# Optimization experiments

Measured on AMD Instinct MI355X. Metric: run time of the kernel, lower is better.

Reference implementation:

```python
import jax, jax.numpy as jnp
import numpy as np


def segment_pool(labels, hidden):
    """Faithful vectorized version of get_entity_embedding_from_hidden_states.

    labels: [B, L] int (0=O, 1=B, 2=I); hidden: [B, L, H].
    Returns [B, L, H]: per-row, the first count_ones(row) slots hold the mean
    hidden state of each mention segment (segments delimited by label==1 over
    the nonzero-label token stream, flattened across the whole batch), rest 0.
    """
    B, L, H = hidden.shape
    N = B * L
    lab = labels.reshape(N)
    h = hidden.reshape(N, H)
    m = lab != 0
    # stable sort: nonzero-label tokens first, original order preserved
    perm = jnp.argsort(jnp.logical_not(m))
    lab_s = lab[perm]
    h_s = h[perm]
    m_s = m[perm]
    b = (lab_s == 1).astype(jnp.int32)
    cum = jnp.cumsum(b)                      # ones seen so far (nonzero stream)
    idx0 = jnp.argmax(b)                     # position of first B-tag (0 if none)
    p = jnp.arange(N)
    # chunk id of nonzero-stream token p: (#ones at positions <= p+idx0) - 1
    seg = cum[jnp.minimum(p + idx0, N - 1)] - 1
    valid = m_s & (seg >= 0)
    seg_ids = jnp.where(valid, seg, N)       # invalid tokens -> dumped segment N
    sums = jax.ops.segment_sum(h_s, seg_ids, num_segments=N + 1)[:N]
    counts = jax.ops.segment_sum(valid.astype(h.dtype), seg_ids, num_segments=N + 1)[:N]
    means = sums / jnp.maximum(counts, 1.0)[:, None]   # [N, H]
    # re-split per row: row b consumes count_ones(b) consecutive means, padded to L
    c = jnp.sum(labels == 1, axis=1)         # [B]
    starts = jnp.cumsum(c) - c               # exclusive prefix sum
    j = jnp.arange(L)
    gidx = jnp.clip(starts[:, None] + j[None, :], 0, N - 1)  # [B, L]
    out = means[gidx]                        # [B, L, H]
    return jnp.where((j[None, :] < c[:, None])[:, :, None], out, jnp.zeros((), hidden.dtype))


def setup_inputs() -> dict:
    key = jax.random.key(0)
    ks = jax.random.split(key, 8)
    B, L, H, E, P = 64, 512, 768, 1000, 300
    return {
        "bio_slot_labels": jax.random.randint(ks[0], (B, L), 0, 3, dtype=jnp.int32),
        "hidden_states": jax.random.normal(ks[1], (B, L, H), dtype=jnp.float32),
        "entity_type_embeddings": jax.random.normal(ks[2], (E, H), dtype=jnp.float32),
        "w1": jax.random.normal(ks[3], (H, H), dtype=jnp.float32) * 0.02,
        "b1": jnp.zeros((H,), dtype=jnp.float32),
        "w2": jax.random.normal(ks[4], (H, 3), dtype=jnp.float32) * 0.02,
        "b2": jnp.zeros((3,), dtype=jnp.float32),
        "w_mention": jax.random.normal(ks[5], (H, P), dtype=jnp.float32) * 0.02,
        "w_desc": jax.random.normal(ks[6], (H, P), dtype=jnp.float32) * 0.02,
    }


def reference(bio_slot_labels, hidden_states, entity_type_embeddings,
              w1, b1, w2, b2, w_mention, w_desc):
    # bio_mlp: Linear -> ReLU -> Linear -> LogSoftmax
    h1 = jax.nn.relu(jnp.einsum('blh,hk->blk', hidden_states, w1) + b1)
    bio_slot_logits = jax.nn.log_softmax(jnp.einsum('blh,hc->blc', h1, w2) + b2, axis=-1)
    predicted_bio_slot = jnp.argmax(bio_slot_logits, axis=-1)

    proj_desc = entity_type_embeddings @ w_desc          # [E, 300]

    def score(labels):
        pooled = segment_pool(labels, hidden_states)     # [B, L, H]
        proj_mention = jnp.einsum('blh,hp->blp', pooled, w_mention)
        dot = jnp.einsum('blp,ep->ble', proj_mention, proj_desc)
        return jax.nn.log_softmax(dot, axis=-1)

    return (bio_slot_logits, score(bio_slot_labels), score(predicted_bio_slot))
```

## Files before the change

kernel.cpp:

```cpp
#include <hip/hip_runtime.h>
#include <stdint.h>

__device__ inline float bf2f(unsigned short u) { return __uint_as_float(((unsigned int)u) << 16); }
__device__ inline unsigned short f2bf(float f) {
    unsigned int x = __float_as_uint(f);
    unsigned int r = x + 0x7fffu + ((x >> 16) & 1u);
    return (unsigned short)(r >> 16);
}

typedef __attribute__((ext_vector_type(8))) short bf16x8;
typedef __attribute__((ext_vector_type(4))) float f32x4;
typedef __attribute__((ext_vector_type(4))) int   v4i;
typedef __attribute__((ext_vector_type(4))) unsigned short u16x4;

#define FLAG_CAP 8192
#define MARGIN 0.02

__device__ inline void gload16(const void* g, void* l) {
    __builtin_amdgcn_global_load_lds(
        (const __attribute__((address_space(1))) void*)g,
        (__attribute__((address_space(3))) void*)l, 16, 0, 0);
}

__global__ __launch_bounds__(256) void gemm_bt(
    const unsigned short* __restrict__ A,
    const unsigned short* __restrict__ Bt,
    void* __restrict__ C,
    const int* __restrict__ Mdev,
    const int* __restrict__ rowMap,
    const float* __restrict__ fb1,
    const float* __restrict__ fw2,
    float* __restrict__ fpart,
    int M, int N, int K, int lda, int ldb, int ldc, int mode, int rowOff,
    size_t zA, int zMeta, int zMap, size_t zC)
{
    int zz = blockIdx.z;
    A += (size_t)zz * zA;
    if (Mdev) M = Mdev[zz * zMeta];
    if (rowMap) rowMap += (size_t)zz * zMap;

    int NT = gridDim.x;
    int p  = blockIdx.x + NT * blockIdx.y;
    int i8 = p >> 3;
    int mt = (p & 7) + 8 * (i8 / NT);
    int nt = i8 % NT;

    if (rowOff + mt * 128 >= M) return;

    __shared__ __align__(16) unsigned short As[128 * 64];
    __shared__ __align__(16) unsigned short Bs[128 * 64];

    int tid  = threadIdx.x;
    int lane = tid & 63, wave = tid >> 6;
    int wRow = (wave >> 1) * 64, wCol = (wave & 1) * 64;
    int mBase = mt * 128, nBase = nt * 128;
    int lm = lane & 15, kg = lane >> 4;
    int sr = tid >> 3;
    int sc = (tid & 7) * 8;

    f32x4 acc[4][4] = {};

    for (int k0 = 0; k0 < K; k0 += 64) {
        __syncthreads();
#pragma unroll
        for (int i = 0; i < 4; ++i) {
            int r = sr + 32 * i;
            int gm = rowOff + mBase + r; if (gm > M - 1) gm = M - 1;
            gload16(&A[(size_t)(gm - rowOff) * lda + k0 + sc], &As[wave * 512 + i * 2048]);
            int gn = nBase + r; if (gn > N - 1) gn = N - 1;
            gload16(&Bt[(size_t)gn * ldb + k0 + sc], &Bs[wave * 512 + i * 2048]);
        }
        __syncthreads();
#pragma unroll
        for (int ks = 0; ks < 2; ++ks) {
            bf16x8 af[4], bfr[4];
#pragma unroll
            for (int i = 0; i < 4; ++i) {
                af[i]  = *(const bf16x8*)&As[(wRow + i * 16 + lm) * 64 + ks * 32 + kg * 8];
                bfr[i] = *(const bf16x8*)&Bs[(wCol + i * 16 + lm) * 64 + ks * 32 + kg * 8];
            }
#pragma unroll
            for (int mi = 0; mi < 4; ++mi)
#pragma unroll
                for (int ni = 0; ni < 4; ++ni)
                    acc[mi][ni] = __builtin_amdgcn_mfma_f32_16x16x32_bf16(
                        af[mi], bfr[ni], acc[mi][ni], 0, 0, 0);
        }
    }

    int rbase = (lane >> 4) * 4;

    if (mode == 3) {
        float b1v[4], w2l[4][3];
#pragma unroll
        for (int ni = 0; ni < 4; ++ni) {
            int n = nBase + wCol + ni * 16 + lm;
            b1v[ni] = fb1[n];
#pragma unroll
            for (int c = 0; c < 3; ++c) w2l[ni][c] = fw2[n * 3 + c];
        }
#pragma unroll
        for (int mi = 0; mi < 4; ++mi) {
            float p2[4][3] = {};
#pragma unroll
            for (int ni = 0; ni < 4; ++ni)
#pragma unroll
                for (int r = 0; r < 4; ++r) {
                    float v = acc[mi][ni][r] + b1v[ni];
                    v = fmaxf(v, 0.f);
                    p2[r][0] += v * w2l[ni][0];
                    p2[r][1] += v * w2l[ni][1];
                    p2[r][2] += v * w2l[ni][2];
                }
#pragma unroll
            for (int r = 0; r < 4; ++r)
#pragma unroll
                for (int c = 0; c < 3; ++c) {
                    float s = p2[r][c];
                    s += __shfl_down(s, 8); s += __shfl_down(s, 4);
                    s += __shfl_down(s, 2); s += __shfl_down(s, 1);
                    p2[r][c] = s;
                }
            if (lm == 0) {
#pragma unroll
                for (int r = 0; r < 4; ++r) {
                    int row = mBase + wRow + mi * 16 + rbase + r;
#pragma unroll
                    for (int c = 0; c < 3; ++c)
                        atomicAdd(&fpart[(size_t)row * 3 + c], p2[r][c]);
                }
            }
        }
        return;
    }

#pragma unroll
    for (int mi = 0; mi < 4; ++mi) {
#pragma unroll
        for (int r = 0; r < 4; ++r) {
            int m = rowOff + mBase + wRow + mi * 16 + rbase + r;
            if (m >= M) continue;
            size_t crow = rowMap ? (size_t)rowMap[m] * ldc : (size_t)(m - rowOff) * ldc;
#pragma unroll
            for (int ni = 0; ni < 4; ++ni) {
                int n = nBase + wCol + ni * 16 + lm;
                if (n >= N) continue;
                float v = acc[mi][ni][r];
                if (mode == 2) ((float*)C)[(size_t)zz * zC + crow + n] = v;
                else           ((unsigned short*)C)[crow + n] = f2bf(v);
            }
        }
    }
}

__global__ __launch_bounds__(256) void prep_all(
    const float* __restrict__ ent, unsigned short* __restrict__ entB,
    const float* __restrict__ hidden, unsigned short* __restrict__ hiddenB,
    const float* __restrict__ wd, unsigned short* __restrict__ wdT,
    const float* __restrict__ w1, unsigned short* __restrict__ w1T,
    const float* __restrict__ wm, unsigned short* __restrict__ wmP,
    v4i* __restrict__ zreg)
{
    __shared__ float tile[32][33];
    int b = blockIdx.x, t = threadIdx.x;
    if (b < 373) {
        int i = b * 256 + t;
        if (i < 95312) { v4i z = {0, 0, 0, 0}; zreg[i] = z; }
        return;
    }
    b -= 373;
    if (b < 750) {
        int i = b * 256 + t;
        float4 v = ((const float4*)ent)[i];
        u16x4 o = { f2bf(v.x), f2bf(v.y), f2bf(v.z), f2bf(v.w) };
        ((u16x4*)entB)[i] = o;
        return;
    }
    b -= 750;
    if (b < 24576) {
        int i = b * 256 + t;
        float4 v = ((const float4*)hidden)[i];
        u16x4 o = { f2bf(v.x), f2bf(v.y), f2bf(v.z), f2bf(v.w) };
        ((u16x4*)hiddenB)[i] = o;
        return;
    }
    b -= 24576;
    if (b < 240 + 576) {
        const float* in; unsigned short* out; int R, C, bx, by;
        if (b < 240) { in = wd; out = wdT; R = 768; C = 300; bx = b % 10; by = b / 10; }
        else { int bb = b - 240; in = w1; out = w1T; R = 768; C = 768; bx = bb % 24; by = bb / 24; }
        int tx = t & 31, ty = t >> 5;
        int c0 = bx * 32, r0 = by * 32;
#pragma unroll
        for (int i = 0; i < 4; ++i) {
            int r = r0 + ty + i * 8, c = c0 + tx;
            if (r < R && c < C) tile[ty + i * 8][tx] = in[(size_t)r * C + c];
        }
        __syncthreads();
#pragma unroll
        for (int i = 0; i < 4; ++i) {
            int orow = c0 + ty + i * 8, ocol = r0 + tx;
            if (orow < C && ocol < R) out[(size_t)orow * R + ocol] = f2bf(tile[tx][ty + i * 8]);
        }
        return;
    }
    b -= 816;
    {
        int idx = b * 256 + t;
        if (idx < 768 * 300) wmP[(size_t)(idx / 300) * 320 + (idx % 300)] = f2bf(wm[idx]);
    }
}

__global__ void bio_final2(const float* __restrict__ part, const float* __restrict__ b2,
                           float* __restrict__ out0, int* __restrict__ predLab,
                           int* __restrict__ flagCnt, int* __restrict__ flagList)
{
    int t = blockIdx.x * 256 + threadIdx.x;
    double a[3];
#pragma unroll
    for (int c = 0; c < 3; ++c) a[c] = (double)part[(size_t)t * 3 + c] + (double)b2[c];
    double mx = a[0]; if (a[1] > mx) mx = a[1]; if (a[2] > mx) mx = a[2];
    double ls = mx + log(exp(a[0] - mx) + exp(a[1] - mx) + exp(a[2] - mx));
    out0[t * 3 + 0] = (float)(a[0] - ls);
    out0[t * 3 + 1] = (float)(a[1] - ls);
    out0[t * 3 + 2] = (float)(a[2] - ls);
    int pbest = 0; double bv = a[0];
    if (a[1] > bv) { bv = a[1]; pbest = 1; }
    if (a[2] > bv) { bv = a[2]; pbest = 2; }
    predLab[t] = pbest;
    double second = -1e300;
#pragma unroll
    for (int c = 0; c < 3; ++c) if (c != pbest && a[c] > second) second = a[c];
    if (bv - second < MARGIN) {
        int i = atomicAdd(flagCnt, 1);
        if (i < FLAG_CAP) flagList[i] = t;
    }
}

__global__ __launch_bounds__(256) void h1_bio_gemm(
    const float* __restrict__ hidden, const int* __restrict__ flagList,
    const float* __restrict__ W,
    const float* __restrict__ b1, const float* __restrict__ w2,
    float* __restrict__ part, const int* __restrict__ Mdev, int partStride)
{
    int M = *Mdev; if (M > FLAG_CAP) M = FLAG_CAP;
    if (M <= 0) return;
    int m0 = blockIdx.x * 64, n0 = blockIdx.y * 64;
    if (m0 >= M) return;
    __shared__ float AsT[16][64];
    __shared__ float Ws[16][64];
    int tx = threadIdx.x, ty = threadIdx.y;
    int tid = ty * 16 + tx;
    float acc[4][4] = {};

    for (int k0 = 0; k0 < 768; k0 += 16) {
        __syncthreads();
        {
            int row = tid >> 2, seg = (tid & 3) * 4;
            int gm = m0 + row; if (gm > M - 1) gm = M - 1;
            float4 v = *(const float4*)&hidden[(size_t)flagList[gm] * 768 + k0 + seg];
            AsT[seg + 0][row] = v.x; AsT[seg + 1][row] = v.y;
            AsT[seg + 2][row] = v.z; AsT[seg + 3][row] = v.w;
        }
        {
            int row = tid >> 4, seg = (tid & 15) * 4;
            *(float4*)&Ws[row][seg] = *(const float4*)&W[(size_t)(k0 + row) * 768 + n0 + seg];
        }
        __syncthreads();
#pragma unroll
        for (int kk = 0; kk < 16; ++kk) {
            float4 av = *(const float4*)&AsT[kk][ty * 4];
            float4 bv = *(const float4*)&Ws[kk][tx * 4];
            float a[4] = {av.x, av.y, av.z, av.w};
            float b[4] = {bv.x, bv.y, bv.z, bv.w};
#pragma unroll
            for (int i = 0; i < 4; ++i)
#pragma unroll
                for (int j = 0; j < 4; ++j)
                    acc[i][j] += a[i] * b[j];
        }
    }

    float b1v[4], w2l[4][3];
#pragma unroll
    for (int j = 0; j < 4; ++j) {
        int n = n0 + tx * 4 + j;
        b1v[j] = b1[n];
#pragma unroll
        for (int c = 0; c < 3; ++c) w2l[j][c] = w2[n * 3 + c];
    }
    float p[4][3] = {};
#pragma unroll
    for (int i = 0; i < 4; ++i)
#pragma unroll
        for (int j = 0; j < 4; ++j) {
            float v = acc[i][j] + b1v[j];
            v = fmaxf(v, 0.f);
#pragma unroll
            for (int c = 0; c < 3; ++c) p[i][c] += v * w2l[j][c];
        }
#pragma unroll
    for (int i = 0; i < 4; ++i)
#pragma unroll
        for (int c = 0; c < 3; ++c) {
            float s = p[i][c];
            s += __shfl_down(s, 8); s += __shfl_down(s, 4);
            s += __shfl_down(s, 2); s += __shfl_down(s, 1);
            p[i][c] = s;
        }
    if (tx == 0) {
#pragma unroll
        for (int i = 0; i < 4; ++i) {
            int t = m0 + ty * 4 + i;
            if (t >= M) continue;
#pragma unroll
            for (int c = 0; c < 3; ++c)
                part[(size_t)blockIdx.y * partStride + (size_t)t * 3 + c] = p[i][c];
        }
    }
}

__global__ __launch_bounds__(1024) void seg_prep2(
    const int* __restrict__ labels, int* predLab,
    int* __restrict__ streamTok, int* __restrict__ cumArr,
    int* __restrict__ meta, int* __restrict__ rowC, int* __restrict__ mapArr,
    int* __restrict__ segFirst,
    const float* __restrict__ partF, const float* __restrict__ b2,
    const int* __restrict__ flagList, const int* __restrict__ flagCnt, int partStride)
{
    int setz = blockIdx.x;
    int t = threadIdx.x;

    if (setz == 1) {
        int cnt = *flagCnt; if (cnt > FLAG_CAP) cnt = FLAG_CAP;
        for (int i = t; i < cnt; i += 1024) {
            double a[3] = {(double)b2[0], (double)b2[1], (double)b2[2]};
#pragma unroll
            for (int blk = 0; blk < 12; ++blk)
#pragma unroll
                for (int c = 0; c < 3; ++c)
                    a[c] += (double)partF[(size_t)blk * partStride + (size_t)i * 3 + c];
            int pbest = 0; double bv = a[0];
            if (a[1] > bv) { bv = a[1]; pbest = 1; }
            if (a[2] > bv) { bv = a[2]; pbest = 2; }
            predLab[flagList[i]] = pbest;
        }
        __syncthreads();
    }

    const int* lab = setz ? predLab : labels;
    int* sTok = streamTok + setz * 32768;
    int* sCum = cumArr + setz * 32768;
    int* mt   = meta + setz * 64;
    int* rC   = rowC + setz * 64;
    int* mp   = mapArr + setz * 32768;
    int* sf   = segFirst + setz * 32768;

    __shared__ int sM[1024], sB[1024];
    __shared__ int sRowC[64], sRowStart[64];
    __shared__ int sIdx0;
    if (t == 0) sIdx0 = 0x7fffffff;
    int base = t * 32;
    int vals[32];
#pragma unroll
    for (int j = 0; j < 8; ++j) {
        v4i v = ((const v4i*)lab)[t * 8 + j];
        vals[4 * j + 0] = v[0]; vals[4 * j + 1] = v[1];
        vals[4 * j + 2] = v[2]; vals[4 * j + 3] = v[3];
    }
    int mc = 0, bc = 0;
#pragma unroll
    for (int i = 0; i < 32; ++i) { mc += (vals[i] != 0); bc += (vals[i] == 1); }
    sM[t] = mc; sB[t] = bc; __syncthreads();
    for (int off = 1; off < 1024; off <<= 1) {
        int vm = 0, vb = 0;
        if (t >= off) { vm = sM[t - off]; vb = sB[t - off]; }
        __syncthreads();
        sM[t] += vm; sB[t] += vb;
        __syncthreads();
    }
    int mBase = sM[t] - mc, bBase = sB[t] - bc;
    int mRun = 0, bRun = 0;
#pragma unroll
    for (int i = 0; i < 32; ++i) {
        int v = vals[i];
        if (v != 0) {
            int q = mBase + mRun;
            sTok[q] = base + i;
            int isB = (v == 1);
            sCum[q] = bBase + bRun + isB;
            if (isB && (bBase + bRun) == 0) sIdx0 = q;
            mRun += 1; bRun += isB;
        }
    }
    if ((t & 15) == 0) sRowStart[t >> 4] = bBase;
    __syncthreads();
    if ((t & 15) == 0) {
        int b = t >> 4;
        sRowC[b] = sB[t + 15] - sRowStart[b];
        rC[b] = sRowC[b];
    }
    if (t == 1023) { mt[0] = sB[1023]; mt[1] = sM[1023]; }
    if (t == 0) mt[2] = (sIdx0 == 0x7fffffff) ? 0 : sIdx0;
    __syncthreads();
    for (int idx = t; idx < 32768; idx += 1024) {
        int b = idx >> 9, j = idx & 511;
        if (j < sRowC[b]) mp[sRowStart[b] + j] = idx;
    }

    int K = sM[1023], numB = sB[1023];
    int idx0 = (sIdx0 == 0x7fffffff) ? 0 : sIdx0;
    for (int q = t; q < K; q += 1024) {
        int qq = q + idx0;
        int c  = (qq < K) ? sCum[qq] : numB;
        int sg = c - 1;
        if (sg < 0) continue;
        int sp = -1;
        if (q > 0) {
            int qq2 = qq - 1;
            int c2  = (qq2 < K) ? sCum[qq2] : numB;
            sp = c2 - 1;
        }
        if (sg != sp) sf[sg] = q;
    }
}

__global__ __launch_bounds__(192) void seg_means2(
    const unsigned short* __restrict__ hiddenB, const int* __restrict__ streamTok,
    const int* __restrict__ segFirst, const int* __restrict__ meta,
    unsigned short* __restrict__ means, size_t zMeans)
{
    int setz = blockIdx.y;
    const int* mt = meta + setz * 64;
    int s = blockIdx.x;
    int numB = mt[0];
    if (s >= numB) return;
    const int* st = streamTok + setz * 32768;
    const int* sf = segFirst + setz * 32768;
    int q0 = sf[s];
    int q1 = (s + 1 < numB) ? sf[s + 1] : mt[1];
    int cnt = q1 - q0;
    int t = threadIdx.x;
    float a0 = 0.f, a1 = 0.f, a2 = 0.f, a3 = 0.f;
    for (int i = 0; i < cnt; ++i) {
        const unsigned short* hr = hiddenB + (size_t)st[q0 + i] * 768;
        u16x4 v = *(const u16x4*)&hr[t * 4];
        a0 += bf2f(v[0]); a1 += bf2f(v[1]); a2 += bf2f(v[2]); a3 += bf2f(v[3]);
    }
    float fc = (float)cnt;
    u16x4 o = { f2bf(a0 / fc), f2bf(a1 / fc), f2bf(a2 / fc), f2bf(a3 / fc) };
    *(u16x4*)&means[(size_t)setz * zMeans + (size_t)s * 768 + t * 4] = o;
}

__global__ __launch_bounds__(256) void softmax_rows2(float* __restrict__ outBase,
                                                     const int* __restrict__ rowCBase,
                                                     size_t zC)
{
    float* out = outBase + (size_t)blockIdx.y * zC;
    const int* rowC = rowCBase + blockIdx.y * 64;
    int v = blockIdx.x;
    int b = v >> 9, j = v & 511;
    int t = threadIdx.x;
    float* row = out + (size_t)v * 1000;
    if (j >= rowC[b]) {
        for (int e = t; e < 1000; e += 256) row[e] = -6.907755278982137f;
        return;
    }
    __shared__ float red[256];
    float x0 = row[t];
    float x1 = row[t + 256];
    float x2 = row[t + 512];
    bool has3 = (t + 768) < 1000;
    float x3 = has3 ? row[t + 768] : -1e30f;
    float mx = fmaxf(fmaxf(x0, x1), fmaxf(x2, x3));
    red[t] = mx; __syncthreads();
    for (int st = 128; st > 0; st >>= 1) { if (t < st) red[t] = fmaxf(red[t], red[t + st]); __syncthreads(); }
    float M = red[0]; __syncthreads();
    float sm = expf(x0 - M) + expf(x1 - M) + expf(x2 - M) + (has3 ? expf(x3 - M) : 0.f);
    red[t] = sm; __syncthreads();
    for (int st = 128; st > 0; st >>= 1) { if (t < st) red[t] += red[t + st]; __syncthreads(); }
    float ls = M + logf(red[0]);
    row[t]       = x0 - ls;
    row[t + 256] = x1 - ls;
    row[t + 512] = x2 - ls;
    if (has3) row[t + 768] = x3 - ls;
}

extern "C" void kernel_launch(void* const* d_in, const int* in_sizes, int n_in,
                              void* d_out, int out_size, void* d_ws, size_t ws_size,
                              hipStream_t stream)
{
    (void)in_sizes; (void)n_in; (void)out_size; (void)ws_size;
    const int*   labels = (const int*)d_in[0];
    const float* hidden = (const float*)d_in[1];
    const float* ent    = (const float*)d_in[2];
    const float* w1     = (const float*)d_in[3];
    const float* b1     = (const float*)d_in[4];
    const float* w2     = (const float*)d_in[5];
    const float* b2     = (const float*)d_in[6];
    const float* wm     = (const float*)d_in[7];
    const float* wd     = (const float*)d_in[8];

    char* ws = (char*)d_ws;
    size_t off = 0;
    auto alloc = [&](size_t bytes) {
        void* p = ws + off;
        off = (off + bytes + 255) & ~(size_t)255;
        return p;
    };
    int* meta      = (int*)alloc(512);
    int* rowC      = (int*)alloc(512);
    int* predLab   = (int*)alloc(32768 * 4);
    int* streamTok = (int*)alloc(2 * 32768 * 4);
    int* cumArr    = (int*)alloc(2 * 32768 * 4);
    int* segFirst  = (int*)alloc(2 * 32768 * 4);
    int* mapArr    = (int*)alloc(2 * 32768 * 4);
    int* flagList  = (int*)alloc(FLAG_CAP * 4);
    unsigned short* entB = (unsigned short*)alloc((size_t)1000 * 768 * 2);
    unsigned short* wdT  = (unsigned short*)alloc((size_t)300 * 768 * 2);
    unsigned short* W2t  = (unsigned short*)alloc((size_t)1000 * 768 * 2);
    unsigned short* w1T  = (unsigned short*)alloc((size_t)768 * 768 * 2);
    unsigned short* hiddenB = (unsigned short*)alloc((size_t)32768 * 768 * 2);
    float* partF = (float*)alloc((size_t)12 * FLAG_CAP * 3 * 4);
    char* zbase = (char*)alloc(1524992);
    unsigned short* pd  = (unsigned short*)zbase;
    unsigned short* wmP = (unsigned short*)(zbase + 640000);
    float* part         = (float*)(zbase + 1131520);
    int* flagCnt        = (int*)(zbase + 1524736);
    unsigned short* means = (unsigned short*)alloc((size_t)2 * 32768 * 768 * 2);

    float* out0 = (float*)d_out;
    float* out1 = out0 + 98304;

    prep_all<<<27415, 256, 0, stream>>>(ent, entB, hidden, hiddenB, wd, wdT,
                                        w1, w1T, wm, wmP, (v4i*)zbase);

    gemm_bt<<<dim3(3, 8), 256, 0, stream>>>(entB, wdT, pd, nullptr, nullptr,
                                            nullptr, nullptr, nullptr,
                                            1000, 300, 768, 768, 768, 320, 0, 0,
                                            0, 0, 0, 0);
    gemm_bt<<<dim3(6, 8), 256, 0, stream>>>(pd, wmP, W2t, nullptr, nullptr,
                                            nullptr, nullptr, nullptr,
                                            1000, 768, 320, 320, 320, 768, 0, 0,
                                            0, 0, 0, 0);

    gemm_bt<<<dim3(6, 256), 256, 0, stream>>>(hiddenB, w1T, nullptr, nullptr, nullptr,
                                              b1, w2, part,
                                              32768, 768, 768, 768, 768, 0, 3, 0,
                                              0, 0, 0, 0);
    bio_final2<<<128, 256, 0, stream>>>(part, b2, out0, predLab, flagCnt, flagList);
    h1_bio_gemm<<<dim3(FLAG_CAP / 64, 12), dim3(16, 16), 0, stream>>>(
        hidden, flagList, w1, b1, w2, partF, flagCnt, FLAG_CAP * 3);

    seg_prep2<<<2, 1024, 0, stream>>>(labels, predLab, streamTok, cumArr, meta, rowC,
                                      mapArr, segFirst, partF, b2, flagList, flagCnt,
                                      FLAG_CAP * 3);
    seg_means2<<<dim3(32768, 2), 192, 0, stream>>>(hiddenB, streamTok, segFirst, meta,
                                                   means, (size_t)32768 * 768);
    gemm_bt<<<dim3(8, 256, 2), 256, 0, stream>>>(means, W2t, out1, meta, mapArr,
                                                 nullptr, nullptr, nullptr,
                                                 0, 1000, 768, 768, 768, 1000, 2, 0,
                                                 (size_t)32768 * 768, 64, 32768,
                                                 (size_t)32768 * 1000);
    softmax_rows2<<<dim3(32768, 2), 256, 0, stream>>>(out1, rowC, (size_t)32768 * 1000);
}
```

Before: 807.7 us.

## Merge independent stages into combined launches with block-range dispatch

```diff
diff --git a/kernel.cpp b/kernel.cpp
--- a/kernel.cpp
+++ b/kernel.cpp
@@ -22,7 +22,7 @@
         (__attribute__((address_space(3))) void*)l, 16, 0, 0);
 }
 
-__global__ __launch_bounds__(256) void gemm_bt(
+static __device__ void dev_gemm(
     const unsigned short* __restrict__ A,
     const unsigned short* __restrict__ Bt,
     void* __restrict__ C,
@@ -31,24 +31,12 @@
     const float* __restrict__ fb1,
     const float* __restrict__ fw2,
     float* __restrict__ fpart,
-    int M, int N, int K, int lda, int ldb, int ldc, int mode, int rowOff,
-    size_t zA, int zMeta, int zMap, size_t zC)
-{
-    int zz = blockIdx.z;
-    A += (size_t)zz * zA;
-    if (Mdev) M = Mdev[zz * zMeta];
-    if (rowMap) rowMap += (size_t)zz * zMap;
-
-    int NT = gridDim.x;
-    int p  = blockIdx.x + NT * blockIdx.y;
-    int i8 = p >> 3;
-    int mt = (p & 7) + 8 * (i8 / NT);
-    int nt = i8 % NT;
-
-    if (rowOff + mt * 128 >= M) return;
-
-    __shared__ __align__(16) unsigned short As[128 * 64];
-    __shared__ __align__(16) unsigned short Bs[128 * 64];
+    int M, int N, int K, int lda, int ldb, int ldc, int mode,
+    int mt, int nt,
+    unsigned short* As, unsigned short* Bs)
+{
+    if (Mdev) M = *Mdev;
+    if (mt * 128 >= M) return;
 
     int tid  = threadIdx.x;
     int lane = tid & 63, wave = tid >> 6;
@@ -65,8 +53,8 @@
 #pragma unroll
         for (int i = 0; i < 4; ++i) {
             int r = sr + 32 * i;
-            int gm = rowOff + mBase + r; if (gm > M - 1) gm = M - 1;
-            gload16(&A[(size_t)(gm - rowOff) * lda + k0 + sc], &As[wave * 512 + i * 2048]);
+            int gm = mBase + r; if (gm > M - 1) gm = M - 1;
+            gload16(&A[(size_t)gm * lda + k0 + sc], &As[wave * 512 + i * 2048]);
             int gn = nBase + r; if (gn > N - 1) gn = N - 1;
             gload16(&Bt[(size_t)gn * ldb + k0 + sc], &Bs[wave * 512 + i * 2048]);
         }
@@ -138,84 +126,116 @@
     for (int mi = 0; mi < 4; ++mi) {
 #pragma unroll
         for (int r = 0; r < 4; ++r) {
-            int m = rowOff + mBase + wRow + mi * 16 + rbase + r;
+            int m = mBase + wRow + mi * 16 + rbase + r;
             if (m >= M) continue;
-            size_t crow = rowMap ? (size_t)rowMap[m] * ldc : (size_t)(m - rowOff) * ldc;
+            size_t crow = rowMap ? (size_t)rowMap[m] * ldc : (size_t)m * ldc;
 #pragma unroll
             for (int ni = 0; ni < 4; ++ni) {
                 int n = nBase + wCol + ni * 16 + lm;
                 if (n >= N) continue;
                 float v = acc[mi][ni][r];
-                if (mode == 2) ((float*)C)[(size_t)zz * zC + crow + n] = v;
+                if (mode == 2) ((float*)C)[crow + n] = v;
                 else           ((unsigned short*)C)[crow + n] = f2bf(v);
             }
         }
     }
 }
 
-__global__ __launch_bounds__(256) void prep_all(
-    const float* __restrict__ ent, unsigned short* __restrict__ entB,
-    const float* __restrict__ hidden, unsigned short* __restrict__ hiddenB,
-    const float* __restrict__ wd, unsigned short* __restrict__ wdT,
-    const float* __restrict__ w1, unsigned short* __restrict__ w1T,
-    const float* __restrict__ wm, unsigned short* __restrict__ wmP,
-    v4i* __restrict__ zreg)
-{
-    __shared__ float tile[32][33];
-    int b = blockIdx.x, t = threadIdx.x;
-    if (b < 373) {
-        int i = b * 256 + t;
-        if (i < 95312) { v4i z = {0, 0, 0, 0}; zreg[i] = z; }
-        return;
-    }
-    b -= 373;
-    if (b < 750) {
-        int i = b * 256 + t;
-        float4 v = ((const float4*)ent)[i];
-        u16x4 o = { f2bf(v.x), f2bf(v.y), f2bf(v.z), f2bf(v.w) };
-        ((u16x4*)entB)[i] = o;
-        return;
-    }
-    b -= 750;
-    if (b < 24576) {
-        int i = b * 256 + t;
-        float4 v = ((const float4*)hidden)[i];
-        u16x4 o = { f2bf(v.x), f2bf(v.y), f2bf(v.z), f2bf(v.w) };
-        ((u16x4*)hiddenB)[i] = o;
-        return;
-    }
-    b -= 24576;
-    if (b < 240 + 576) {
-        const float* in; unsigned short* out; int R, C, bx, by;
-        if (b < 240) { in = wd; out = wdT; R = 768; C = 300; bx = b % 10; by = b / 10; }
-        else { int bb = b - 240; in = w1; out = w1T; R = 768; C = 768; bx = bb % 24; by = bb / 24; }
-        int tx = t & 31, ty = t >> 5;
-        int c0 = bx * 32, r0 = by * 32;
-#pragma unroll
-        for (int i = 0; i < 4; ++i) {
-            int r = r0 + ty + i * 8, c = c0 + tx;
-            if (r < R && c < C) tile[ty + i * 8][tx] = in[(size_t)r * C + c];
-        }
-        __syncthreads();
-#pragma unroll
-        for (int i = 0; i < 4; ++i) {
-            int orow = c0 + ty + i * 8, ocol = r0 + tx;
-            if (orow < C && ocol < R) out[(size_t)orow * R + ocol] = f2bf(tile[tx][ty + i * 8]);
-        }
-        return;
-    }
-    b -= 816;
-    {
-        int idx = b * 256 + t;
-        if (idx < 768 * 300) wmP[(size_t)(idx / 300) * 320 + (idx % 300)] = f2bf(wm[idx]);
-    }
-}
-
-__global__ void bio_final2(const float* __restrict__ part, const float* __restrict__ b2,
-                           float* __restrict__ out0, int* __restrict__ predLab,
-                           int* __restrict__ flagCnt, int* __restrict__ flagList)
-{
-    int t = blockIdx.x * 256 + threadIdx.x;
+static __device__ void dev_scan(const int* __restrict__ lab,
+    int* __restrict__ sTok, int* __restrict__ sCum, int* __restrict__ mt,
+    int* __restrict__ rC, int* __restrict__ mp, int* __restrict__ sf,
+    int* sM, int* sB, int* sRS, int* sRC, int* sIdx)
+{
+    int t = threadIdx.x;
+    if (t == 0) sIdx[0] = 0x7fffffff;
+    int mc = 0, bc = 0;
+#pragma unroll
+    for (int j = 0; j < 32; ++j) {
+        v4i v = ((const v4i*)lab)[t * 32 + j];
+#pragma unroll
+        for (int e = 0; e < 4; ++e) { mc += (v[e] != 0); bc += (v[e] == 1); }
+    }
+    sM[t] = mc; sB[t] = bc; __syncthreads();
+    for (int off = 1; off < 256; off <<= 1) {
+        int vm = 0, vb = 0;
+        if (t >= off) { vm = sM[t - off]; vb = sB[t - off]; }
+        __syncthreads();
+        sM[t] += vm; sB[t] += vb;
+        __syncthreads();
+    }
+    int mBase = sM[t] - mc, bBase = sB[t] - bc;
+    int mRun = 0, bRun = 0;
+    int base = t * 128;
+    for (int j = 0; j < 32; ++j) {
+        v4i v = ((const v4i*)lab)[t * 32 + j];
+#pragma unroll
+        for (int e = 0; e < 4; ++e) {
+            int val = v[e];
+            if (val != 0) {
+                int q = mBase + mRun;
+                sTok[q] = base + j * 4 + e;
+                int isB = (val == 1);
+                sCum[q] = bBase + bRun + isB;
+                if (isB && (bBase + bRun) == 0) sIdx[0] = q;
+                mRun += 1; bRun += isB;
+            }
+        }
+    }
+    if ((t & 3) == 0) sRS[t >> 2] = bBase;
+    __syncthreads();
+    if ((t & 3) == 0) {
+        int b = t >> 2;
+        sRC[b] = sB[4 * b + 3] - sRS[b];
+        rC[b] = sRC[b];
+    }
+    if (t == 255) { mt[0] = sB[255]; mt[1] = sM[255]; }
+    if (t == 0) mt[2] = (sIdx[0] == 0x7fffffff) ? 0 : sIdx[0];
+    __syncthreads();
+    for (int idx = t; idx < 32768; idx += 256) {
+        int b = idx >> 9, j = idx & 511;
+        if (j < sRC[b]) mp[sRS[b] + j] = idx;
+    }
+    int K = sM[255], numB = sB[255];
+    int idx0 = (sIdx[0] == 0x7fffffff) ? 0 : sIdx[0];
+    for (int q = t; q < K; q += 256) {
+        int qq = q + idx0;
+        int c  = (qq < K) ? sCum[qq] : numB;
+        int sg = c - 1;
+        if (sg < 0) continue;
+        int sp = -1;
+        if (q > 0) {
+            int qq2 = qq - 1;
+            int c2  = (qq2 < K) ? sCum[qq2] : numB;
+            sp = c2 - 1;
+        }
+        if (sg != sp) sf[sg] = q;
+    }
+}
+
+static __device__ void dev_fix(const float* __restrict__ partF, const float* __restrict__ b2,
+                               const int* __restrict__ flagList, const int* __restrict__ flagCnt,
+                               int* __restrict__ predLab, int partStride)
+{
+    int cnt = *flagCnt; if (cnt > FLAG_CAP) cnt = FLAG_CAP;
+    for (int i = threadIdx.x; i < cnt; i += 256) {
+        double a[3] = {(double)b2[0], (double)b2[1], (double)b2[2]};
+#pragma unroll
+        for (int blk = 0; blk < 12; ++blk)
+#pragma unroll
+            for (int c = 0; c < 3; ++c)
+                a[c] += (double)partF[(size_t)blk * partStride + (size_t)i * 3 + c];
+        int pbest = 0; double bv = a[0];
+        if (a[1] > bv) { bv = a[1]; pbest = 1; }
+        if (a[2] > bv) { bv = a[2]; pbest = 2; }
+        predLab[flagList[i]] = pbest;
+    }
+}
+
+static __device__ void dev_final2(int t, const float* __restrict__ part,
+                                  const float* __restrict__ b2,
+                                  float* __restrict__ out0, int* __restrict__ predLab,
+                                  int* __restrict__ flagCnt, int* __restrict__ flagList)
+{
     double a[3];
 #pragma unroll
     for (int c = 0; c < 3; ++c) a[c] = (double)part[(size_t)t * 3 + c] + (double)b2[c];
@@ -237,40 +257,39 @@
     }
 }
 
-__global__ __launch_bounds__(256) void h1_bio_gemm(
+static __device__ void dev_h1(int bxm, int byn,
     const float* __restrict__ hidden, const int* __restrict__ flagList,
     const float* __restrict__ W,
     const float* __restrict__ b1, const float* __restrict__ w2,
-    float* __restrict__ part, const int* __restrict__ Mdev, int partStride)
+    float* __restrict__ part, const int* __restrict__ Mdev, int partStride,
+    float* AsT, float* Ws)
 {
     int M = *Mdev; if (M > FLAG_CAP) M = FLAG_CAP;
     if (M <= 0) return;
-    int m0 = blockIdx.x * 64, n0 = blockIdx.y * 64;
+    int m0 = bxm * 64, n0 = byn * 64;
     if (m0 >= M) return;
-    __shared__ float AsT[16][64];
-    __shared__ float Ws[16][64];
-    int tx = threadIdx.x, ty = threadIdx.y;
-    int tid = ty * 16 + tx;
+    int t = threadIdx.x;
+    int tx = t & 15, ty = t >> 4;
     float acc[4][4] = {};
 
     for (int k0 = 0; k0 < 768; k0 += 16) {
         __syncthreads();
         {
-            int row = tid >> 2, seg = (tid & 3) * 4;
+            int row = t >> 2, seg = (t & 3) * 4;
             int gm = m0 + row; if (gm > M - 1) gm = M - 1;
             float4 v = *(const float4*)&hidden[(size_t)flagList[gm] * 768 + k0 + seg];
-            AsT[seg + 0][row] = v.x; AsT[seg + 1][row] = v.y;
-            AsT[seg + 2][row] = v.z; AsT[seg + 3][row] = v.w;
+            AsT[(seg + 0) * 64 + row] = v.x; AsT[(seg + 1) * 64 + row] = v.y;
+            AsT[(seg + 2) * 64 + row] = v.z; AsT[(seg + 3) * 64 + row] = v.w;
         }
         {
-            int row = tid >> 4, seg = (tid & 15) * 4;
-            *(float4*)&Ws[row][seg] = *(const float4*)&W[(size_t)(k0 + row) * 768 + n0 + seg];
+            int row = t >> 4, seg = (t & 15) * 4;
+            *(float4*)&Ws[row * 64 + seg] = *(const float4*)&W[(size_t)(k0 + row) * 768 + n0 + seg];
         }
         __syncthreads();
 #pragma unroll
         for (int kk = 0; kk < 16; ++kk) {
-            float4 av = *(const float4*)&AsT[kk][ty * 4];
-            float4 bv = *(const float4*)&Ws[kk][tx * 4];
+            float4 av = *(const float4*)&AsT[kk * 64 + ty * 4];
+            float4 bv = *(const float4*)&Ws[kk * 64 + tx * 4];
             float a[4] = {av.x, av.y, av.z, av.w};
             float b[4] = {bv.x, bv.y, bv.z, bv.w};
 #pragma unroll
@@ -311,136 +330,26 @@
     if (tx == 0) {
 #pragma unroll
         for (int i = 0; i < 4; ++i) {
-            int t = m0 + ty * 4 + i;
-            if (t >= M) continue;
+            int tt = m0 + ty * 4 + i;
+            if (tt >= M) continue;
 #pragma unroll
             for (int c = 0; c < 3; ++c)
-                part[(size_t)blockIdx.y * partStride + (size_t)t * 3 + c] = p[i][c];
-        }
-    }
-}
-
-__global__ __launch_bounds__(1024) void seg_prep2(
-    const int* __restrict__ labels, int* predLab,
-    int* __restrict__ streamTok, int* __restrict__ cumArr,
-    int* __restrict__ meta, int* __restrict__ rowC, int* __restrict__ mapArr,
-    int* __restrict__ segFirst,
-    const float* __restrict__ partF, const float* __restrict__ b2,
-    const int* __restrict__ flagList, const int* __restrict__ flagCnt, int partStride)
-{
-    int setz = blockIdx.x;
-    int t = threadIdx.x;
-
-    if (setz == 1) {
-        int cnt = *flagCnt; if (cnt > FLAG_CAP) cnt = FLAG_CAP;
-        for (int i = t; i < cnt; i += 1024) {
-            double a[3] = {(double)b2[0], (double)b2[1], (double)b2[2]};
-#pragma unroll
-            for (int blk = 0; blk < 12; ++blk)
-#pragma unroll
-                for (int c = 0; c < 3; ++c)
-                    a[c] += (double)partF[(size_t)blk * partStride + (size_t)i * 3 + c];
-            int pbest = 0; double bv = a[0];
-            if (a[1] > bv) { bv = a[1]; pbest = 1; }
-            if (a[2] > bv) { bv = a[2]; pbest = 2; }
-            predLab[flagList[i]] = pbest;
-        }
-        __syncthreads();
-    }
-
-    const int* lab = setz ? predLab : labels;
-    int* sTok = streamTok + setz * 32768;
-    int* sCum = cumArr + setz * 32768;
-    int* mt   = meta + setz * 64;
-    int* rC   = rowC + setz * 64;
-    int* mp   = mapArr + setz * 32768;
-    int* sf   = segFirst + setz * 32768;
-
-    __shared__ int sM[1024], sB[1024];
-    __shared__ int sRowC[64], sRowStart[64];
-    __shared__ int sIdx0;
-    if (t == 0) sIdx0 = 0x7fffffff;
-    int base = t * 32;
-    int vals[32];
-#pragma unroll
-    for (int j = 0; j < 8; ++j) {
-        v4i v = ((const v4i*)lab)[t * 8 + j];
-        vals[4 * j + 0] = v[0]; vals[4 * j + 1] = v[1];
-        vals[4 * j + 2] = v[2]; vals[4 * j + 3] = v[3];
-    }
-    int mc = 0, bc = 0;
-#pragma unroll
-    for (int i = 0; i < 32; ++i) { mc += (vals[i] != 0); bc += (vals[i] == 1); }
-    sM[t] = mc; sB[t] = bc; __syncthreads();
-    for (int off = 1; off < 1024; off <<= 1) {
-        int vm = 0, vb = 0;
-        if (t >= off) { vm = sM[t - off]; vb = sB[t - off]; }
-        __syncthreads();
-        sM[t] += vm; sB[t] += vb;
-        __syncthreads();
-    }
-    int mBase = sM[t] - mc, bBase = sB[t] - bc;
-    int mRun = 0, bRun = 0;
-#pragma unroll
-    for (int i = 0; i < 32; ++i) {
-        int v = vals[i];
-        if (v != 0) {
-            int q = mBase + mRun;
-            sTok[q] = base + i;
-            int isB = (v == 1);
-            sCum[q] = bBase + bRun + isB;
-            if (isB && (bBase + bRun) == 0) sIdx0 = q;
-            mRun += 1; bRun += isB;
-        }
-    }
-    if ((t & 15) == 0) sRowStart[t >> 4] = bBase;
-    __syncthreads();
-    if ((t & 15) == 0) {
-        int b = t >> 4;
-        sRowC[b] = sB[t + 15] - sRowStart[b];
-        rC[b] = sRowC[b];
-    }
-    if (t == 1023) { mt[0] = sB[1023]; mt[1] = sM[1023]; }
-    if (t == 0) mt[2] = (sIdx0 == 0x7fffffff) ? 0 : sIdx0;
-    __syncthreads();
-    for (int idx = t; idx < 32768; idx += 1024) {
-        int b = idx >> 9, j = idx & 511;
-        if (j < sRowC[b]) mp[sRowStart[b] + j] = idx;
-    }
-
-    int K = sM[1023], numB = sB[1023];
-    int idx0 = (sIdx0 == 0x7fffffff) ? 0 : sIdx0;
-    for (int q = t; q < K; q += 1024) {
-        int qq = q + idx0;
-        int c  = (qq < K) ? sCum[qq] : numB;
-        int sg = c - 1;
-        if (sg < 0) continue;
-        int sp = -1;
-        if (q > 0) {
-            int qq2 = qq - 1;
-            int c2  = (qq2 < K) ? sCum[qq2] : numB;
-            sp = c2 - 1;
-        }
-        if (sg != sp) sf[sg] = q;
-    }
-}
-
-__global__ __launch_bounds__(192) void seg_means2(
-    const unsigned short* __restrict__ hiddenB, const int* __restrict__ streamTok,
-    const int* __restrict__ segFirst, const int* __restrict__ meta,
-    unsigned short* __restrict__ means, size_t zMeans)
-{
-    int setz = blockIdx.y;
-    const int* mt = meta + setz * 64;
-    int s = blockIdx.x;
+                part[(size_t)byn * partStride + (size_t)tt * 3 + c] = p[i][c];
+        }
+    }
+}
+
+static __device__ void dev_means(int s, const unsigned short* __restrict__ hiddenB,
+                                 const int* __restrict__ st, const int* __restrict__ sf,
+                                 const int* __restrict__ mt, unsigned short* __restrict__ meansSet)
+{
     int numB = mt[0];
     if (s >= numB) return;
-    const int* st = streamTok + setz * 32768;
-    const int* sf = segFirst + setz * 32768;
+    int t = threadIdx.x;
+    if (t >= 192) return;
     int q0 = sf[s];
     int q1 = (s + 1 < numB) ? sf[s + 1] : mt[1];
     int cnt = q1 - q0;
-    int t = threadIdx.x;
     float a0 = 0.f, a1 = 0.f, a2 = 0.f, a3 = 0.f;
     for (int i = 0; i < cnt; ++i) {
         const unsigned short* hr = hiddenB + (size_t)st[q0 + i] * 768;
@@ -449,16 +358,12 @@
     }
     float fc = (float)cnt;
     u16x4 o = { f2bf(a0 / fc), f2bf(a1 / fc), f2bf(a2 / fc), f2bf(a3 / fc) };
-    *(u16x4*)&means[(size_t)setz * zMeans + (size_t)s * 768 + t * 4] = o;
-}
-
-__global__ __launch_bounds__(256) void softmax_rows2(float* __restrict__ outBase,
-                                                     const int* __restrict__ rowCBase,
-                                                     size_t zC)
-{
-    float* out = outBase + (size_t)blockIdx.y * zC;
-    const int* rowC = rowCBase + blockIdx.y * 64;
-    int v = blockIdx.x;
+    *(u16x4*)&meansSet[(size_t)s * 768 + t * 4] = o;
+}
+
+static __device__ void dev_softmax(int v, float* __restrict__ out,
+                                   const int* __restrict__ rowC, float* red)
+{
     int b = v >> 9, j = v & 511;
     int t = threadIdx.x;
     float* row = out + (size_t)v * 1000;
@@ -466,7 +371,6 @@
         for (int e = t; e < 1000; e += 256) row[e] = -6.907755278982137f;
         return;
     }
-    __shared__ float red[256];
     float x0 = row[t];
     float x1 = row[t + 256];
     float x2 = row[t + 512];
@@ -484,6 +388,187 @@
     row[t + 256] = x1 - ls;
     row[t + 512] = x2 - ls;
     if (has3) row[t + 768] = x3 - ls;
+}
+
+
+__global__ __launch_bounds__(256) void k_prep(
+    const float* __restrict__ ent, unsigned short* __restrict__ entB,
+    const float* __restrict__ hidden, unsigned short* __restrict__ hiddenB,
+    const float* __restrict__ wd, unsigned short* __restrict__ wdT,
+    const float* __restrict__ w1, unsigned short* __restrict__ w1T,
+    const float* __restrict__ wm, unsigned short* __restrict__ wmP,
+    v4i* __restrict__ zreg,
+    const int* __restrict__ labels, int* streamTok, int* cumArr, int* meta,
+    int* rowC, int* mapArr, int* segFirst)
+{
+    __shared__ float tile[32][33];
+    __shared__ int sM[256], sB[256], sRS[64], sRC[64], sIdx[1];
+    int b = blockIdx.x, t = threadIdx.x;
+    if (b == 0) {
+        dev_scan(labels, streamTok, cumArr, meta, rowC, mapArr, segFirst,
+                 sM, sB, sRS, sRC, sIdx);
+        return;
+    }
+    b -= 1;
+    if (b < 373) {
+        int i = b * 256 + t;
+        if (i < 95312) { v4i z = {0, 0, 0, 0}; zreg[i] = z; }
+        return;
+    }
+    b -= 373;
+    if (b < 750) {
+        int i = b * 256 + t;
+        float4 v = ((const float4*)ent)[i];
+        u16x4 o = { f2bf(v.x), f2bf(v.y), f2bf(v.z), f2bf(v.w) };
+        ((u16x4*)entB)[i] = o;
+        return;
+    }
+    b -= 750;
+    if (b < 24576) {
+        int i = b * 256 + t;
+        float4 v = ((const float4*)hidden)[i];
+        u16x4 o = { f2bf(v.x), f2bf(v.y), f2bf(v.z), f2bf(v.w) };
+        ((u16x4*)hiddenB)[i] = o;
+        return;
+    }
+    b -= 24576;
+    if (b < 240 + 576) {
+        const float* in; unsigned short* out; int R, C, bx, by;
+        if (b < 240) { in = wd; out = wdT; R = 768; C = 300; bx = b % 10; by = b / 10; }
+        else { int bb = b - 240; in = w1; out = w1T; R = 768; C = 768; bx = bb % 24; by = bb / 24; }
+        int tx = t & 31, ty = t >> 5;
+        int c0 = bx * 32, r0 = by * 32;
+#pragma unroll
+        for (int i = 0; i < 4; ++i) {
+            int r = r0 + ty + i * 8, c = c0 + tx;
+            if (r < R && c < C) tile[ty + i * 8][tx] = in[(size_t)r * C + c];
+        }
+        __syncthreads();
+#pragma unroll
+        for (int i = 0; i < 4; ++i) {
+            int orow = c0 + ty + i * 8, ocol = r0 + tx;
+            if (orow < C && ocol < R) out[(size_t)orow * R + ocol] = f2bf(tile[tx][ty + i * 8]);
+        }
+        return;
+    }
+    b -= 816;
+    {
+        int idx = b * 256 + t;
+        if (idx < 768 * 300) wmP[(size_t)(idx / 300) * 320 + (idx % 300)] = f2bf(wm[idx]);
+    }
+}
+
+__global__ __launch_bounds__(256) void k_l2(
+    const unsigned short* __restrict__ hiddenB, const unsigned short* __restrict__ w1T,
+    const float* __restrict__ b1, const float* __restrict__ w2, float* __restrict__ part,
+    const unsigned short* __restrict__ entB, const unsigned short* __restrict__ wdT,
+    unsigned short* __restrict__ pd,
+    const int* __restrict__ streamTok, const int* __restrict__ segFirst,
+    const int* __restrict__ meta, unsigned short* __restrict__ means)
+{
+    __shared__ __align__(16) unsigned short As[128 * 64];
+    __shared__ __align__(16) unsigned short Bs[128 * 64];
+    int bx = blockIdx.x;
+    if (bx < 1536) {
+        dev_gemm(hiddenB, w1T, nullptr, nullptr, nullptr, b1, w2, part,
+                 32768, 768, 768, 768, 768, 0, 3, bx / 6, bx % 6, As, Bs);
+        return;
+    }
+    bx -= 1536;
+    if (bx < 24) {
+        dev_gemm(entB, wdT, pd, nullptr, nullptr, nullptr, nullptr, nullptr,
+                 1000, 300, 768, 768, 768, 320, 0, bx / 3, bx % 3, As, Bs);
+        return;
+    }
+    bx -= 24;
+    dev_means(bx, hiddenB, streamTok, segFirst, meta, means);
+}
+
+__global__ __launch_bounds__(256) void k_l3(
+    const float* __restrict__ part, const float* __restrict__ b2,
+    float* __restrict__ out0, int* __restrict__ predLab,
+    int* __restrict__ flagCnt, int* __restrict__ flagList,
+    const unsigned short* __restrict__ pd, const unsigned short* __restrict__ wmP,
+    unsigned short* __restrict__ W2t)
+{
+    __shared__ __align__(16) unsigned short As[128 * 64];
+    __shared__ __align__(16) unsigned short Bs[128 * 64];
+    int bx = blockIdx.x;
+    if (bx < 128) {
+        dev_final2(bx * 256 + threadIdx.x, part, b2, out0, predLab, flagCnt, flagList);
+        return;
+    }
+    bx -= 128;
+    dev_gemm(pd, wmP, W2t, nullptr, nullptr, nullptr, nullptr, nullptr,
+             1000, 768, 320, 320, 320, 768, 0, bx / 6, bx % 6, As, Bs);
+}
+
+__global__ __launch_bounds__(256) void k_l4(
+    const float* __restrict__ hidden, const int* __restrict__ flagList,
+    const float* __restrict__ w1, const float* __restrict__ b1,
+    const float* __restrict__ w2, float* __restrict__ partF, const int* __restrict__ flagCnt,
+    const unsigned short* __restrict__ means, const unsigned short* __restrict__ W2t,
+    float* __restrict__ out1, const int* __restrict__ meta, const int* __restrict__ mapArr)
+{
+    __shared__ __align__(16) char smem[32768];
+    int bx = blockIdx.x;
+    if (bx < 1536) {
+        dev_h1(bx % 128, bx / 128, hidden, flagList, w1, b1, w2, partF, flagCnt,
+               FLAG_CAP * 3, (float*)smem, (float*)(smem + 4096));
+        return;
+    }
+    bx -= 1536;
+    dev_gemm(means, W2t, out1, meta, mapArr, nullptr, nullptr, nullptr,
+             0, 1000, 768, 768, 768, 1000, 2, bx / 8, bx % 8,
+             (unsigned short*)smem, (unsigned short*)(smem + 16384));
+}
+
+__global__ __launch_bounds__(256) void k_l5(
+    float* __restrict__ out1, int* __restrict__ rowC,
+    int* __restrict__ predLab, int* __restrict__ streamTok, int* __restrict__ cumArr,
+    int* __restrict__ meta, int* __restrict__ mapArr, int* __restrict__ segFirst,
+    const float* __restrict__ partF, const float* __restrict__ b2,
+    const int* __restrict__ flagList, const int* __restrict__ flagCnt)
+{
+    __shared__ float red[256];
+    __shared__ int sM[256], sB[256], sRS[64], sRC[64], sIdx[1];
+    int bx = blockIdx.x;
+    if (bx == 0) {
+        dev_fix(partF, b2, flagList, flagCnt, predLab, FLAG_CAP * 3);
+        __syncthreads();
+        dev_scan(predLab, streamTok + 32768, cumArr + 32768, meta + 64, rowC + 64,
+                 mapArr + 32768, segFirst + 32768, sM, sB, sRS, sRC, sIdx);
+        return;
+    }
+    dev_softmax(bx - 1, out1, rowC, red);
+}
+
+__global__ __launch_bounds__(256) void k_means1(
+    const unsigned short* __restrict__ hiddenB, const int* __restrict__ streamTok,
+    const int* __restrict__ segFirst, const int* __restrict__ meta,
+    unsigned short* __restrict__ means)
+{
+    dev_means(blockIdx.x, hiddenB, streamTok + 32768, segFirst + 32768, meta + 64,
+              means + (size_t)32768 * 768);
+}
+
+__global__ __launch_bounds__(256) void k_gemm1(
+    const unsigned short* __restrict__ means, const unsigned short* __restrict__ W2t,
+    float* __restrict__ out2, const int* __restrict__ meta, const int* __restrict__ mapArr)
+{
+    __shared__ __align__(16) unsigned short As[128 * 64];
+    __shared__ __align__(16) unsigned short Bs[128 * 64];
+    int bx = blockIdx.x;
+    dev_gemm(means + (size_t)32768 * 768, W2t, out2, meta + 64, mapArr + 32768,
+             nullptr, nullptr, nullptr,
+             0, 1000, 768, 768, 768, 1000, 2, bx / 8, bx % 8, As, Bs);
+}
+
+__global__ __launch_bounds__(256) void k_soft1(
+    float* __restrict__ out2, const int* __restrict__ rowC)
+{
+    __shared__ float red[256];
+    dev_softmax(blockIdx.x, out2, rowC + 64, red);
 }
 
 extern "C" void kernel_launch(void* const* d_in, const int* in_sizes, int n_in,
@@ -531,36 +616,23 @@
 
     float* out0 = (float*)d_out;
     float* out1 = out0 + 98304;
-
-    prep_all<<<27415, 256, 0, stream>>>(ent, entB, hidden, hiddenB, wd, wdT,
-                                        w1, w1T, wm, wmP, (v4i*)zbase);
-
-    gemm_bt<<<dim3(3, 8), 256, 0, stream>>>(entB, wdT, pd, nullptr, nullptr,
-                                            nullptr, nullptr, nullptr,
-                                            1000, 300, 768, 768, 768, 320, 0, 0,
-                                            0, 0, 0, 0);
-    gemm_bt<<<dim3(6, 8), 256, 0, stream>>>(pd, wmP, W2t, nullptr, nullptr,
-                                            nullptr, nullptr, nullptr,
-                                            1000, 768, 320, 320, 320, 768, 0, 0,
-                                            0, 0, 0, 0);
-
-    gemm_bt<<<dim3(6, 256), 256, 0, stream>>>(hiddenB, w1T, nullptr, nullptr, nullptr,
-                                              b1, w2, part,
-                                              32768, 768, 768, 768, 768, 0, 3, 0,
-                                              0, 0, 0, 0);
-    bio_final2<<<128, 256, 0, stream>>>(part, b2, out0, predLab, flagCnt, flagList);
-    h1_bio_gemm<<<dim3(FLAG_CAP / 64, 12), dim3(16, 16), 0, stream>>>(
-        hidden, flagList, w1, b1, w2, partF, flagCnt, FLAG_CAP * 3);
-
-    seg_prep2<<<2, 1024, 0, stream>>>(labels, predLab, streamTok, cumArr, meta, rowC,
-                                      mapArr, segFirst, partF, b2, flagList, flagCnt,
-                                      FLAG_CAP * 3);
-    seg_means2<<<dim3(32768, 2), 192, 0, stream>>>(hiddenB, streamTok, segFirst, meta,
-                                                   means, (size_t)32768 * 768);
-    gemm_bt<<<dim3(8, 256, 2), 256, 0, stream>>>(means, W2t, out1, meta, mapArr,
-                                                 nullptr, nullptr, nullptr,
-                                                 0, 1000, 768, 768, 768, 1000, 2, 0,
-                                                 (size_t)32768 * 768, 64, 32768,
-                                                 (size_t)32768 * 1000);
-    softmax_rows2<<<dim3(32768, 2), 256, 0, stream>>>(out1, rowC, (size_t)32768 * 1000);
-}
+    float* out2 = out1 + (size_t)32768 * 1000;
+
+    k_prep<<<27416, 256, 0, stream>>>(ent, entB, hidden, hiddenB, wd, wdT,
+                                      w1, w1T, wm, wmP, (v4i*)zbase,
+                                      labels, streamTok, cumArr, meta, rowC,
+                                      mapArr, segFirst);
+    k_l2<<<1536 + 24 + 32768, 256, 0, stream>>>(hiddenB, w1T, b1, w2, part,
+                                                entB, wdT, pd,
+                                                streamTok, segFirst, meta, means);
+    k_l3<<<128 + 48, 256, 0, stream>>>(part, b2, out0, predLab, flagCnt, flagList,
+                                       pd, wmP, W2t);
+    k_l4<<<1536 + 2048, 256, 0, stream>>>(hidden, flagList, w1, b1, w2, partF, flagCnt,
+                                          means, W2t, out1, meta, mapArr);
+    k_l5<<<1 + 32768, 256, 0, stream>>>(out1, rowC, predLab, streamTok, cumArr,
+                                        meta, mapArr, segFirst,
+                                        partF, b2, flagList, flagCnt);
+    k_means1<<<32768, 256, 0, stream>>>(hiddenB, streamTok, segFirst, meta, means);
+    k_gemm1<<<2048, 256, 0, stream>>>(means, W2t, out2, meta, mapArr);
+    k_soft1<<<32768, 256, 0, stream>>>(out2, rowC);
+}
```

New measurement: 1.139 ms. 41.0% more time.

## Pack four segments per block in seg_means, drop gemm tile swizzle

Applied to the files above, without the earlier changes.

```diff
diff --git a/kernel.cpp b/kernel.cpp
--- a/kernel.cpp
+++ b/kernel.cpp
@@ -39,12 +39,7 @@
     if (Mdev) M = Mdev[zz * zMeta];
     if (rowMap) rowMap += (size_t)zz * zMap;
 
-    int NT = gridDim.x;
-    int p  = blockIdx.x + NT * blockIdx.y;
-    int i8 = p >> 3;
-    int mt = (p & 7) + 8 * (i8 / NT);
-    int nt = i8 % NT;
-
+    int nt = blockIdx.x, mt = blockIdx.y;
     if (rowOff + mt * 128 >= M) return;
 
     __shared__ __align__(16) unsigned short As[128 * 64];
@@ -249,8 +244,8 @@
     if (m0 >= M) return;
     __shared__ float AsT[16][64];
     __shared__ float Ws[16][64];
-    int tx = threadIdx.x, ty = threadIdx.y;
-    int tid = ty * 16 + tx;
+    int tx = threadIdx.x & 15, ty = threadIdx.x >> 4;
+    int tid = threadIdx.x;
     float acc[4][4] = {};
 
     for (int k0 = 0; k0 < 768; k0 += 16) {
@@ -425,31 +420,40 @@
     }
 }
 
-__global__ __launch_bounds__(192) void seg_means2(
+__global__ __launch_bounds__(256) void seg_means2(
     const unsigned short* __restrict__ hiddenB, const int* __restrict__ streamTok,
     const int* __restrict__ segFirst, const int* __restrict__ meta,
     unsigned short* __restrict__ means, size_t zMeans)
 {
     int setz = blockIdx.y;
     const int* mt = meta + setz * 64;
-    int s = blockIdx.x;
     int numB = mt[0];
+    int s = blockIdx.x * 4 + (threadIdx.x >> 6);
     if (s >= numB) return;
+    int lane = threadIdx.x & 63;
     const int* st = streamTok + setz * 32768;
     const int* sf = segFirst + setz * 32768;
     int q0 = sf[s];
     int q1 = (s + 1 < numB) ? sf[s + 1] : mt[1];
     int cnt = q1 - q0;
-    int t = threadIdx.x;
-    float a0 = 0.f, a1 = 0.f, a2 = 0.f, a3 = 0.f;
+    float a[12] = {};
     for (int i = 0; i < cnt; ++i) {
         const unsigned short* hr = hiddenB + (size_t)st[q0 + i] * 768;
-        u16x4 v = *(const u16x4*)&hr[t * 4];
-        a0 += bf2f(v[0]); a1 += bf2f(v[1]); a2 += bf2f(v[2]); a3 += bf2f(v[3]);
+#pragma unroll
+        for (int p = 0; p < 3; ++p) {
+            u16x4 v = *(const u16x4*)&hr[(p * 64 + lane) * 4];
+            a[p * 4 + 0] += bf2f(v[0]); a[p * 4 + 1] += bf2f(v[1]);
+            a[p * 4 + 2] += bf2f(v[2]); a[p * 4 + 3] += bf2f(v[3]);
+        }
     }
     float fc = (float)cnt;
-    u16x4 o = { f2bf(a0 / fc), f2bf(a1 / fc), f2bf(a2 / fc), f2bf(a3 / fc) };
-    *(u16x4*)&means[(size_t)setz * zMeans + (size_t)s * 768 + t * 4] = o;
+    unsigned short* o = means + (size_t)setz * zMeans + (size_t)s * 768;
+#pragma unroll
+    for (int p = 0; p < 3; ++p) {
+        u16x4 ov = { f2bf(a[p * 4 + 0] / fc), f2bf(a[p * 4 + 1] / fc),
+                     f2bf(a[p * 4 + 2] / fc), f2bf(a[p * 4 + 3] / fc) };
+        *(u16x4*)&o[(p * 64 + lane) * 4] = ov;
+    }
 }
 
 __global__ __launch_bounds__(256) void softmax_rows2(float* __restrict__ outBase,
@@ -549,14 +553,14 @@
                                               32768, 768, 768, 768, 768, 0, 3, 0,
                                               0, 0, 0, 0);
     bio_final2<<<128, 256, 0, stream>>>(part, b2, out0, predLab, flagCnt, flagList);
-    h1_bio_gemm<<<dim3(FLAG_CAP / 64, 12), dim3(16, 16), 0, stream>>>(
+    h1_bio_gemm<<<dim3(FLAG_CAP / 64, 12), dim3(256), 0, stream>>>(
         hidden, flagList, w1, b1, w2, partF, flagCnt, FLAG_CAP * 3);
 
     seg_prep2<<<2, 1024, 0, stream>>>(labels, predLab, streamTok, cumArr, meta, rowC,
                                       mapArr, segFirst, partF, b2, flagList, flagCnt,
                                       FLAG_CAP * 3);
-    seg_means2<<<dim3(32768, 2), 192, 0, stream>>>(hiddenB, streamTok, segFirst, meta,
-                                                   means, (size_t)32768 * 768);
+    seg_means2<<<dim3(8192, 2), 256, 0, stream>>>(hiddenB, streamTok, segFirst, meta,
+                                                  means, (size_t)32768 * 768);
     gemm_bt<<<dim3(8, 256, 2), 256, 0, stream>>>(means, W2t, out1, meta, mapArr,
                                                  nullptr, nullptr, nullptr,
                                                  0, 1000, 768, 768, 768, 1000, 2, 0,
```

Measured after the change: 802.2 us. Within noise of the previous version (-0.7%).
